# Performance work log

Hardware: AMD Instinct MI355X
Metric: run time of the kernel (lower is better)

## Reference

```python
import jax, jax.numpy as jnp
import numpy as np


def setup_inputs() -> dict:
    key = jax.random.key(0)
    k1, k2, k3, k4 = jax.random.split(key, 4)
    B, H, L, R, DV = 4, 8, 2048, 8, 128  # rank R=8 is hard-coded in the module
    return {
        "v": jax.random.normal(k1, (B, H, L, DV), dtype=jnp.float32),
        "random_attn_1": jax.random.normal(k2, (B, H, L, R), dtype=jnp.float32),
        "random_attn_2": jax.random.normal(k3, (B, H, R, L), dtype=jnp.float32),
        "mask": jax.random.randint(k4, (B, 1, L, L), 0, 2).astype(jnp.int32),
        "len_q": 2048,
    }


def reference(v, random_attn_1, random_attn_2, mask, len_q):
    B = mask.shape[0]
    # low-rank score matrix: [B,H,Lq,8] @ [B,H,8,Lq] -> [B,H,Lq,Lq]
    a1 = random_attn_1[:B, :, :len_q, :]
    a2 = random_attn_2[:B, :, :, :len_q]
    scores = jnp.einsum('bhlr,bhrm->bhlm', a1, a2)
    # masked_fill(mask == 0, -1e9)
    scores = jnp.where(mask == 0, jnp.float32(-1e9), scores)
    attn = jax.nn.softmax(scores, axis=-1)  # dropout = identity (eval mode)
    out = jnp.einsum('bhlm,bhmd->bhld', attn, v)
    return out, attn
```

## Files before the change

### kernel.cpp

```cpp
#include <hip/hip_runtime.h>

#define L 2048
#define RNK 8
#define DV 128
#define NBH 32

typedef float  f32x4 __attribute__((ext_vector_type(4)));
typedef int    i32x4 __attribute__((ext_vector_type(4)));
typedef short  s16x8 __attribute__((ext_vector_type(8)));
typedef short  s16x4 __attribute__((ext_vector_type(4)));

__device__ __forceinline__ short f2bf(float f) {
    union { float f; unsigned u; } x; x.f = f;
    unsigned r = x.u + 0x7fffu + ((x.u >> 16) & 1u);
    return (short)(r >> 16);
}

__global__ __launch_bounds__(256) void softmax_kernel(
    const float* __restrict__ a1,
    const float* __restrict__ a2,
    const int*   __restrict__ mask,
    float*       __restrict__ attn)
{
    const int lane = threadIdx.x & 63;
    const int wv   = threadIdx.x >> 6;
    const long row0 = (long)blockIdx.x * 32 + (long)wv * 8;

    for (int it = 0; it < 8; ++it) {
        const long row = row0 + it;
        const int bh = (int)(row >> 11);
        const int l  = (int)(row & (L - 1));
        const int b  = bh >> 3;

        const float* a1p = a1 + ((long)bh * L + l) * RNK;
        float a1v[RNK];
#pragma unroll
        for (int r = 0; r < RNK; ++r) a1v[r] = a1p[r];

        const float* a2p = a2 + (long)bh * RNK * L;
        const int*   mp  = mask + ((long)b * L + l) * L;

        float s[8][4];
#pragma unroll
        for (int j = 0; j < 8; ++j) {
            const int c = j * 256 + lane * 4;
            f32x4 sc;
            sc[0] = 0.f; sc[1] = 0.f; sc[2] = 0.f; sc[3] = 0.f;
#pragma unroll
            for (int r = 0; r < RNK; ++r) {
                const f32x4 av = *(const f32x4*)(a2p + (long)r * L + c);
#pragma unroll
                for (int q = 0; q < 4; ++q) sc[q] += a1v[r] * av[q];
            }
            const i32x4 mm = *(const i32x4*)(mp + c);
#pragma unroll
            for (int q = 0; q < 4; ++q)
                s[j][q] = (mm[q] == 0) ? -1e9f : sc[q];
        }

        float mx = s[0][0];
#pragma unroll
        for (int j = 0; j < 8; ++j)
#pragma unroll
            for (int q = 0; q < 4; ++q) mx = fmaxf(mx, s[j][q]);
#pragma unroll
        for (int d = 1; d < 64; d <<= 1) mx = fmaxf(mx, __shfl_xor(mx, d, 64));

        float sum = 0.f;
#pragma unroll
        for (int j = 0; j < 8; ++j)
#pragma unroll
            for (int q = 0; q < 4; ++q) {
                const float e = __expf(s[j][q] - mx);
                s[j][q] = e;
                sum += e;
            }
#pragma unroll
        for (int d = 1; d < 64; d <<= 1) sum += __shfl_xor(sum, d, 64);

        const float inv = 1.f / sum;
        float* op = attn + (long)row * L;
#pragma unroll
        for (int j = 0; j < 8; ++j) {
            f32x4 o;
#pragma unroll
            for (int q = 0; q < 4; ++q) o[q] = s[j][q] * inv;
            *(f32x4*)(op + j * 256 + lane * 4) = o;
        }
    }
}

#define BK 64
#define SA 72

__global__ __launch_bounds__(256) void pv_kernel(
    const float* __restrict__ attn,
    const float* __restrict__ v,
    float*       __restrict__ out)
{
    __shared__ short As[128 * SA];
    __shared__ short Vs[DV * SA];

    const int t    = threadIdx.x;
    const int lane = t & 63;
    const int wv   = t >> 6;
    const int wr   = wv >> 1;
    const int wc   = wv & 1;
    const int bh   = blockIdx.y;
    const int mt   = blockIdx.x;

    const float* Ag = attn + (size_t)bh * L * L + (size_t)mt * 128 * L;
    const float* Vg = v    + (size_t)bh * L * DV;

    f32x4 acc[4][4];
#pragma unroll
    for (int m = 0; m < 4; ++m)
#pragma unroll
        for (int n = 0; n < 4; ++n)
#pragma unroll
            for (int i = 0; i < 4; ++i) acc[m][n][i] = 0.f;

    const int ar = t >> 4;
    const int ak = (t & 15) * 4;
    const int vd = (t & 31) * 4;
    const int vk = (t >> 5) * 8;

    for (int k0 = 0; k0 < L; k0 += BK) {
#pragma unroll
        for (int p = 0; p < 8; ++p) {
            const int rrow = p * 16 + ar;
            const f32x4 f = *(const f32x4*)(Ag + (size_t)rrow * L + k0 + ak);
            s16x4 pk;
#pragma unroll
            for (int q = 0; q < 4; ++q) pk[q] = f2bf(f[q]);
            *(s16x4*)(As + rrow * SA + ak) = pk;
        }
        f32x4 vv[8];
#pragma unroll
        for (int j = 0; j < 8; ++j)
            vv[j] = *(const f32x4*)(Vg + (size_t)(k0 + vk + j) * DV + vd);
#pragma unroll
        for (int c = 0; c < 4; ++c) {
            s16x8 pk;
#pragma unroll
            for (int j = 0; j < 8; ++j) pk[j] = f2bf(vv[j][c]);
            *(s16x8*)(Vs + (vd + c) * SA + vk) = pk;
        }
        __syncthreads();

#pragma unroll
        for (int kk = 0; kk < 2; ++kk) {
            const int kb = kk * 32 + (lane >> 4) * 8;
            s16x8 af[4], bf[4];
#pragma unroll
            for (int m = 0; m < 4; ++m)
                af[m] = *(const s16x8*)(As + (wr * 64 + m * 16 + (lane & 15)) * SA + kb);
#pragma unroll
            for (int n = 0; n < 4; ++n)
                bf[n] = *(const s16x8*)(Vs + (wc * 64 + n * 16 + (lane & 15)) * SA + kb);
#pragma unroll
            for (int m = 0; m < 4; ++m)
#pragma unroll
                for (int n = 0; n < 4; ++n)
                    acc[m][n] = __builtin_amdgcn_mfma_f32_16x16x32_bf16(
                        af[m], bf[n], acc[m][n], 0, 0, 0);
        }
        __syncthreads();
    }

    float* Og = out + (size_t)bh * L * DV + (size_t)mt * 128 * DV;
#pragma unroll
    for (int m = 0; m < 4; ++m)
#pragma unroll
        for (int n = 0; n < 4; ++n)
#pragma unroll
            for (int i = 0; i < 4; ++i) {
                const int rrow = wr * 64 + m * 16 + (lane >> 4) * 4 + i;
                const int col  = wc * 64 + n * 16 + (lane & 15);
                Og[(size_t)rrow * DV + col] = acc[m][n][i];
            }
}

extern "C" void kernel_launch(void* const* d_in, const int* in_sizes, int n_in,
                              void* d_out, int out_size, void* d_ws, size_t ws_size,
                              hipStream_t stream) {
    const float* v    = (const float*)d_in[0];
    const float* a1   = (const float*)d_in[1];
    const float* a2   = (const float*)d_in[2];
    const int*   mask = (const int*)d_in[3];

    float* out  = (float*)d_out;
    float* attn = out + (size_t)NBH * L * DV;

    softmax_kernel<<<2048, 256, 0, stream>>>(a1, a2, mask, attn);
    pv_kernel<<<dim3(16, NBH), 256, 0, stream>>>(attn, v, out);
}
```

Baseline: 1.037 ms.

## Emit bf16 attention copy in softmax and feed PV GEMM via direct LDS loads

The softmax kernel now handles one row per 256-thread block and, besides the fp32 attention output, writes a bf16 copy into the workspace. A new kernel pre-transposes V to bf16, so the PV GEMM can stream already-converted tiles straight into LDS with global_load_lds and skip the per-tile fp32 read and conversion. This cuts PV's read traffic of the large attention matrix in half, at the cost of an extra bf16 write of that matrix plus one more launch. If the workspace is too small, the old fp32 path is used instead.

```diff
diff --git a/kernel.cpp b/kernel.cpp
--- a/kernel.cpp
+++ b/kernel.cpp
@@ -5,10 +5,11 @@
 #define DV 128
 #define NBH 32
 
-typedef float  f32x4 __attribute__((ext_vector_type(4)));
-typedef int    i32x4 __attribute__((ext_vector_type(4)));
-typedef short  s16x8 __attribute__((ext_vector_type(8)));
-typedef short  s16x4 __attribute__((ext_vector_type(4)));
+typedef float         f32x4 __attribute__((ext_vector_type(4)));
+typedef int           i32x4 __attribute__((ext_vector_type(4)));
+typedef short         s16x8 __attribute__((ext_vector_type(8)));
+typedef short         s16x4 __attribute__((ext_vector_type(4)));
+typedef unsigned int  u32;
 
 __device__ __forceinline__ short f2bf(float f) {
     union { float f; unsigned u; } x; x.f = f;
@@ -16,83 +17,199 @@
     return (short)(r >> 16);
 }
 
-__global__ __launch_bounds__(256) void softmax_kernel(
+__global__ __launch_bounds__(256, 4) void softmax_kernel2(
     const float* __restrict__ a1,
     const float* __restrict__ a2,
     const int*   __restrict__ mask,
-    float*       __restrict__ attn)
+    float*       __restrict__ attn,
+    short*       __restrict__ attn_bf)
 {
-    const int lane = threadIdx.x & 63;
-    const int wv   = threadIdx.x >> 6;
-    const long row0 = (long)blockIdx.x * 32 + (long)wv * 8;
-
-    for (int it = 0; it < 8; ++it) {
-        const long row = row0 + it;
-        const int bh = (int)(row >> 11);
-        const int l  = (int)(row & (L - 1));
-        const int b  = bh >> 3;
-
-        const float* a1p = a1 + ((long)bh * L + l) * RNK;
-        float a1v[RNK];
-#pragma unroll
-        for (int r = 0; r < RNK; ++r) a1v[r] = a1p[r];
-
-        const float* a2p = a2 + (long)bh * RNK * L;
-        const int*   mp  = mask + ((long)b * L + l) * L;
-
-        float s[8][4];
-#pragma unroll
-        for (int j = 0; j < 8; ++j) {
-            const int c = j * 256 + lane * 4;
-            f32x4 sc;
-            sc[0] = 0.f; sc[1] = 0.f; sc[2] = 0.f; sc[3] = 0.f;
-#pragma unroll
-            for (int r = 0; r < RNK; ++r) {
-                const f32x4 av = *(const f32x4*)(a2p + (long)r * L + c);
-#pragma unroll
-                for (int q = 0; q < 4; ++q) sc[q] += a1v[r] * av[q];
+    __shared__ float red[8];
+    const int t   = threadIdx.x;
+    const long row = blockIdx.x;
+    const int bh = (int)(row >> 11);
+    const int l  = (int)(row & (L - 1));
+    const int b  = bh >> 3;
+
+    const float* a1p = a1 + ((long)bh * L + l) * RNK;
+    float a1v[RNK];
+    {
+        const f32x4 u = *(const f32x4*)a1p;
+        const f32x4 w = *(const f32x4*)(a1p + 4);
+#pragma unroll
+        for (int q = 0; q < 4; ++q) { a1v[q] = u[q]; a1v[4 + q] = w[q]; }
+    }
+    const float* a2p = a2 + (long)bh * RNK * L;
+    const int*   mp  = mask + ((long)b * L + l) * L;
+
+    float s[2][4];
+#pragma unroll
+    for (int h = 0; h < 2; ++h) {
+        const int c = h * 1024 + t * 4;
+        f32x4 sc;
+        sc[0] = 0.f; sc[1] = 0.f; sc[2] = 0.f; sc[3] = 0.f;
+#pragma unroll
+        for (int r = 0; r < RNK; ++r) {
+            const f32x4 av = *(const f32x4*)(a2p + (long)r * L + c);
+#pragma unroll
+            for (int q = 0; q < 4; ++q) sc[q] += a1v[r] * av[q];
+        }
+        const i32x4 mm = *(const i32x4*)(mp + c);
+#pragma unroll
+        for (int q = 0; q < 4; ++q)
+            s[h][q] = (mm[q] == 0) ? -1e9f : sc[q];
+    }
+
+    float mx = s[0][0];
+#pragma unroll
+    for (int h = 0; h < 2; ++h)
+#pragma unroll
+        for (int q = 0; q < 4; ++q) mx = fmaxf(mx, s[h][q]);
+#pragma unroll
+    for (int d = 1; d < 64; d <<= 1) mx = fmaxf(mx, __shfl_xor(mx, d, 64));
+    if ((t & 63) == 0) red[t >> 6] = mx;
+    __syncthreads();
+    mx = fmaxf(fmaxf(red[0], red[1]), fmaxf(red[2], red[3]));
+
+    float sum = 0.f;
+#pragma unroll
+    for (int h = 0; h < 2; ++h)
+#pragma unroll
+        for (int q = 0; q < 4; ++q) {
+            const float e = __expf(s[h][q] - mx);
+            s[h][q] = e;
+            sum += e;
+        }
+#pragma unroll
+    for (int d = 1; d < 64; d <<= 1) sum += __shfl_xor(sum, d, 64);
+    if ((t & 63) == 0) red[4 + (t >> 6)] = sum;
+    __syncthreads();
+    sum = (red[4] + red[5]) + (red[6] + red[7]);
+    const float inv = 1.f / sum;
+
+    float* op = attn + (long)row * L;
+#pragma unroll
+    for (int h = 0; h < 2; ++h) {
+        const int c = h * 1024 + t * 4;
+        f32x4 o;
+#pragma unroll
+        for (int q = 0; q < 4; ++q) o[q] = s[h][q] * inv;
+        *(f32x4*)(op + c) = o;
+        if (attn_bf) {
+            s16x4 pk;
+#pragma unroll
+            for (int q = 0; q < 4; ++q) pk[q] = f2bf(o[q]);
+            *(s16x4*)(attn_bf + (long)row * L + c) = pk;
+        }
+    }
+}
+
+__global__ __launch_bounds__(256, 4) void vt_convert(
+    const float* __restrict__ v, short* __restrict__ vt)
+{
+    __shared__ short T[DV][72];
+    const int bh = blockIdx.y;
+    const int k0 = blockIdx.x * 64;
+    const int t  = threadIdx.x;
+
+    const float* src = v + (size_t)bh * L * DV;
+    const int kr = t >> 5;
+    const int dc = (t & 31) * 4;
+#pragma unroll
+    for (int p = 0; p < 8; ++p) {
+        const int k = p * 8 + kr;
+        const f32x4 f = *(const f32x4*)(src + (size_t)(k0 + k) * DV + dc);
+#pragma unroll
+        for (int q = 0; q < 4; ++q) T[dc + q][k] = f2bf(f[q]);
+    }
+    __syncthreads();
+
+    short* dst = vt + (size_t)bh * DV * L;
+    const int dr = t >> 1;
+    const int kc = (t & 1) * 32;
+#pragma unroll
+    for (int j = 0; j < 4; ++j)
+        *(s16x8*)(dst + (size_t)dr * L + k0 + kc + j * 8) =
+            *(const s16x8*)(&T[dr][kc + j * 8]);
+}
+
+__global__ __launch_bounds__(256, 2) void pv_bf16(
+    const short* __restrict__ attn_bf,
+    const short* __restrict__ vt,
+    float*       __restrict__ out)
+{
+    __shared__ short As[128 * 64];
+    __shared__ short Vs[128 * 64];
+
+    const int t    = threadIdx.x;
+    const int lane = t & 63;
+    const int wv   = t >> 6;
+    const int wr   = wv >> 1;
+    const int wc   = wv & 1;
+    const int bh   = blockIdx.y;
+    const int mt   = blockIdx.x;
+
+    const short* Ab = attn_bf + ((size_t)bh * L + (size_t)mt * 128) * L;
+    const short* Vb = vt + (size_t)bh * DV * L;
+
+    f32x4 acc[4][4];
+#pragma unroll
+    for (int m = 0; m < 4; ++m)
+#pragma unroll
+        for (int n = 0; n < 4; ++n)
+#pragma unroll
+            for (int i = 0; i < 4; ++i) acc[m][n][i] = 0.f;
+
+    const int sr = t >> 3;
+    const int sc = (t & 7) * 8;
+
+    for (int k0 = 0; k0 < L; k0 += 64) {
+#pragma unroll
+        for (int p = 0; p < 4; ++p) {
+            const int row = p * 32 + sr;
+            __builtin_amdgcn_global_load_lds(
+                (const u32*)(Ab + (size_t)row * L + k0 + sc),
+                (u32*)(As + row * 64 + sc), 16, 0, 0);
+            __builtin_amdgcn_global_load_lds(
+                (const u32*)(Vb + (size_t)row * L + k0 + sc),
+                (u32*)(Vs + row * 64 + sc), 16, 0, 0);
+        }
+        __syncthreads();
+
+#pragma unroll
+        for (int kk = 0; kk < 2; ++kk) {
+            const int kb = kk * 32 + (lane >> 4) * 8;
+            s16x8 af[4], bf[4];
+#pragma unroll
+            for (int m = 0; m < 4; ++m)
+                af[m] = *(const s16x8*)(As + (wr * 64 + m * 16 + (lane & 15)) * 64 + kb);
+#pragma unroll
+            for (int n = 0; n < 4; ++n)
+                bf[n] = *(const s16x8*)(Vs + (wc * 64 + n * 16 + (lane & 15)) * 64 + kb);
+#pragma unroll
+            for (int m = 0; m < 4; ++m)
+#pragma unroll
+                for (int n = 0; n < 4; ++n)
+                    acc[m][n] = __builtin_amdgcn_mfma_f32_16x16x32_bf16(
+                        af[m], bf[n], acc[m][n], 0, 0, 0);
+        }
+        __syncthreads();
+    }
+
+    float* Og = out + (size_t)bh * L * DV + (size_t)mt * 128 * DV;
+#pragma unroll
+    for (int m = 0; m < 4; ++m)
+#pragma unroll
+        for (int n = 0; n < 4; ++n)
+#pragma unroll
+            for (int i = 0; i < 4; ++i) {
+                const int rrow = wr * 64 + m * 16 + (lane >> 4) * 4 + i;
+                const int col  = wc * 64 + n * 16 + (lane & 15);
+                Og[(size_t)rrow * DV + col] = acc[m][n][i];
             }
-            const i32x4 mm = *(const i32x4*)(mp + c);
-#pragma unroll
-            for (int q = 0; q < 4; ++q)
-                s[j][q] = (mm[q] == 0) ? -1e9f : sc[q];
-        }
-
-        float mx = s[0][0];
-#pragma unroll
-        for (int j = 0; j < 8; ++j)
-#pragma unroll
-            for (int q = 0; q < 4; ++q) mx = fmaxf(mx, s[j][q]);
-#pragma unroll
-        for (int d = 1; d < 64; d <<= 1) mx = fmaxf(mx, __shfl_xor(mx, d, 64));
-
-        float sum = 0.f;
-#pragma unroll
-        for (int j = 0; j < 8; ++j)
-#pragma unroll
-            for (int q = 0; q < 4; ++q) {
-                const float e = __expf(s[j][q] - mx);
-                s[j][q] = e;
-                sum += e;
-            }
-#pragma unroll
-        for (int d = 1; d < 64; d <<= 1) sum += __shfl_xor(sum, d, 64);
-
-        const float inv = 1.f / sum;
-        float* op = attn + (long)row * L;
-#pragma unroll
-        for (int j = 0; j < 8; ++j) {
-            f32x4 o;
-#pragma unroll
-            for (int q = 0; q < 4; ++q) o[q] = s[j][q] * inv;
-            *(f32x4*)(op + j * 256 + lane * 4) = o;
-        }
-    }
-}
-
-#define BK 64
+}
+
 #define SA 72
-
 __global__ __launch_bounds__(256) void pv_kernel(
     const float* __restrict__ attn,
     const float* __restrict__ v,
@@ -125,7 +242,7 @@
     const int vd = (t & 31) * 4;
     const int vk = (t >> 5) * 8;
 
-    for (int k0 = 0; k0 < L; k0 += BK) {
+    for (int k0 = 0; k0 < L; k0 += 64) {
 #pragma unroll
         for (int p = 0; p < 8; ++p) {
             const int rrow = p * 16 + ar;
@@ -192,6 +309,18 @@
     float* out  = (float*)d_out;
     float* attn = out + (size_t)NBH * L * DV;
 
-    softmax_kernel<<<2048, 256, 0, stream>>>(a1, a2, mask, attn);
-    pv_kernel<<<dim3(16, NBH), 256, 0, stream>>>(attn, v, out);
-}
+    const size_t ATTN_BF_BYTES = (size_t)NBH * L * L * 2;
+    const size_t VT_BYTES      = (size_t)NBH * DV * L * 2;
+    const bool use_ws = (ws_size >= ATTN_BF_BYTES + VT_BYTES);
+
+    short* attn_bf = use_ws ? (short*)d_ws : nullptr;
+    short* vt      = use_ws ? (short*)((char*)d_ws + ATTN_BF_BYTES) : nullptr;
+
+    softmax_kernel2<<<65536, 256, 0, stream>>>(a1, a2, mask, attn, attn_bf);
+    if (use_ws) {
+        vt_convert<<<dim3(32, NBH), 256, 0, stream>>>(v, vt);
+        pv_bf16<<<dim3(16, NBH), 256, 0, stream>>>(attn_bf, vt, out);
+    } else {
+        pv_kernel<<<dim3(16, NBH), 256, 0, stream>>>(attn, v, out);
+    }
+}
```

New measurement: 885.0 us. 14.6% less time.
